# Kernel tuning notes

Measured on AMD Instinct MI355X. Metric: run time of the kernel, lower is better.

The kernel has to match this reference:

```python
import jax, jax.numpy as jnp
import numpy as np


def _conv(x, w, padding):
    # x: NCHW, w: OIHW
    return jax.lax.conv_general_dilated(
        x, w, window_strides=(1, 1), padding=padding,
        dimension_numbers=('NCHW', 'OIHW', 'NCHW'))


def setup_inputs() -> dict:
    key = jax.random.key(0)
    ks = jax.random.split(key, 4)
    B, Cin, H, W = 128, 1024, 14, 14
    planes, expansion = 256, 4
    x = jax.random.normal(ks[0], (B, Cin, H, W), dtype=jnp.float32)
    # conv weights (layouts are fully dense since rho=0.0)
    w1 = jax.random.normal(ks[1], (planes, Cin, 1, 1), dtype=jnp.float32) * 0.02
    w2 = jax.random.normal(ks[2], (planes, planes, 3, 3), dtype=jnp.float32) * 0.02
    w3 = jax.random.normal(ks[3], (planes * expansion, planes, 1, 1), dtype=jnp.float32) * 0.02
    # Fixup scalar biases / scale
    z = jnp.zeros((1,), dtype=jnp.float32)
    return {
        'x': x, 'w1': w1, 'w2': w2, 'w3': w3,
        'bias1b': z, 'bias2a': z, 'bias2b': z, 'bias3a': z, 'bias3b': z,
        'rscale': jnp.ones((1,), dtype=jnp.float32), 'rbias': z,
    }


def reference(x, w1, w2, w3, bias1b, bias2a, bias2b, bias3a, bias3b, rscale, rbias):
    # conv1(x) + bias1b  (1x1, fused output bias)
    out = _conv(x, w1, 'VALID') + bias1b[0]
    # conv2(out + bias2a) + bias2b  (3x3, pad 1, fused input+output bias)
    out = _conv(out + bias2a[0], w2, 'SAME') + bias2b[0]
    # conv3(out + bias3a) + bias3b  (1x1)
    out = _conv(out + bias3a[0], w3, 'VALID') + bias3b[0]
    # fused scale + bias + residual ReLU: relu(out*rscale + rbias + identity)
    return jax.nn.relu(out * rscale[0] + rbias[0] + x)
```

## Files before the change

kernel.cpp:

```cpp
#include <hip/hip_runtime.h>
#include <stdint.h>

typedef __bf16 bf16x8 __attribute__((ext_vector_type(8)));
typedef float f32x4 __attribute__((ext_vector_type(4)));
typedef unsigned short u16;

__device__ __forceinline__ u16 f2bf(float f){
  uint32_t u = __float_as_uint(f);
  u = (u + 0x7fffu + ((u >> 16) & 1u)) >> 16;
  return (u16)u;
}
__device__ __forceinline__ float bf2f(u16 v){
  return __uint_as_float(((uint32_t)v) << 16);
}
__device__ __forceinline__ void gl_lds16(const void* g, void* l){
  __builtin_amdgcn_global_load_lds((const __attribute__((address_space(1))) void*)g,
                                   (__attribute__((address_space(3))) void*)l, 16, 0, 0);
}

__global__ __launch_bounds__(256) void prep_all(
    const float* __restrict__ w1, const float* __restrict__ w2,
    const float* __restrict__ w3, u16* __restrict__ wb1, u16* __restrict__ wb2,
    u16* __restrict__ wb3, u16* __restrict__ xp1){
  int bid = blockIdx.x, t = threadIdx.x;
  if (bid < 1024){
    int i = bid*256 + t; wb1[i] = f2bf(w1[i]);
  } else if (bid < 3328){
    int i = (bid-1024)*256 + t;
    int o = i / 2304, r = i - o*2304, kq = r >> 8, c = r & 255;
    wb2[i] = f2bf(w2[((size_t)o*256 + c)*9 + kq]);
  } else if (bid < 4352){
    int i = (bid-3328)*256 + t; wb3[i] = f2bf(w3[i]);
  } else {
    int tid = (bid-4352)*256 + t;
    int row_i = tid >> 5, w = tid & 31;
    unsigned b = (unsigned)row_i / 60u, k = (unsigned)row_i - b*60u;
    int y, xx;
    if (k < 32){ y = (k>>4)*15; xx = k & 15; }
    else if (k < 46){ y = k - 31; xx = 0; }
    else { y = k - 45; xx = 15; }
    size_t row = (size_t)b*256 + y*16 + xx;
    ((ulonglong2*)(xp1 + row*256))[w] = (ulonglong2){0,0};
  }
}

__global__ __launch_bounds__(256) void transform_x(const float* __restrict__ x,
                                                   u16* __restrict__ xp0){
  __shared__ float lds[64*201];
  const int b = blockIdx.y, c0 = blockIdx.x*64, t = threadIdx.x;
  const float4* src = (const float4*)x + (size_t)b*50176 + (size_t)c0*49;
  #pragma unroll
  for (int r = 0; r < 13; ++r){
    int q = r*256 + t;
    if (q < 3136){
      unsigned c = (unsigned)q / 49u, f = (unsigned)q - c*49u;
      float4 v = src[q];
      float* d = &lds[c*201 + f*4];
      d[0]=v.x; d[1]=v.y; d[2]=v.z; d[3]=v.w;
    }
  }
  __syncthreads();
  const int c4 = (t & 15)*4, pg = t >> 4;
  #pragma unroll
  for (int r = 0; r < 13; ++r){
    int p = r*16 + pg;
    if (p < 196){
      ushort4 pk;
      ((u16*)&pk)[0] = f2bf(lds[(c4+0)*201 + p]);
      ((u16*)&pk)[1] = f2bf(lds[(c4+1)*201 + p]);
      ((u16*)&pk)[2] = f2bf(lds[(c4+2)*201 + p]);
      ((u16*)&pk)[3] = f2bf(lds[(c4+3)*201 + p]);
      *(ushort4*)&xp0[((size_t)b*196 + p)*1024 + c0 + c4] = pk;
    }
  }
}

template<int CID>
__device__ __forceinline__ void gemm_body(
    const u16* __restrict__ A, const u16* __restrict__ B,
    u16* __restrict__ Obf, float* __restrict__ Of32, const u16* __restrict__ xresb,
    const float* __restrict__ s0, const float* __restrict__ s1, const float* __restrict__ s2)
{
  constexpr int KTOT  = (CID==1) ? 1024 : (CID==2) ? 2304 : 256;
  constexpr int NSTEP = KTOT / 64;
  constexpr int BN    = (CID==3) ? 128 : 64;
  constexpr int WN    = (CID==3) ? 64 : 32;
  constexpr int NJ    = WN / 16;
  constexpr int NBG   = BN*8/256;
  constexpr int BUFB  = 16384 + BN*128;
  constexpr int LDSZ  = (CID==3) ? 33792 : 2*BUFB;

  __shared__ char lds[LDSZ];
  const int t    = threadIdx.x;
  const int lane = t & 63;
  const int w    = t >> 6;
  const int wm   = (w >> 1) * 64, wn = (w & 1) * WN;

  const int orig = blockIdx.x;
  const int bid  = (orig & 7) * ((int)gridDim.x >> 3) + (orig >> 3);
  int n0, m0;
  if constexpr (CID==3){ n0 = (bid >> 3) * 128; m0 = (bid & 7) * 128; }
  else                 { n0 = (bid >> 1) * 64;  m0 = (bid & 1) * 128; }

  f32x4 acc[4][NJ] = {};

  uint32_t aoff[4], boff[NBG];
  #pragma unroll
  for (int i = 0; i < 4; ++i){
    int gl = i*256 + t, row = gl >> 3, ss = gl & 7;
    int xo = (ss ^ (row & 7)) << 4;
    aoff[i] = (uint32_t)(m0 + row) * (KTOT*2) + xo;
  }
  #pragma unroll
  for (int i = 0; i < NBG; ++i){
    int gl = i*256 + t, row = gl >> 3, ss = gl & 7;
    int xo = (ss ^ (row & 7)) << 4;
    uint32_t n = n0 + row;
    if constexpr (CID==1)      boff[i] = n * 2048u + xo;
    else if constexpr (CID==3) boff[i] = n * 512u + xo;
    else {
      uint32_t b = n / 196u, p = n - b*196u;
      uint32_t py = p / 14u,  px = p - py*14u;
      uint32_t prow = b*256u + (py+1)*16u + (px+1);
      boff[i] = prow * 512u + xo;
    }
  }

  auto stage = [&](int buf, int s){
    char* Ab = lds + buf*BUFB;
    char* Bb = Ab + 16384;
    const int ka = s*128;
    int kb;
    if constexpr (CID==2){
      int kq = s >> 2;
      kb = ((kq/3 - 1)*16 + (kq%3) - 1)*512 + (s & 3)*128;
    } else kb = ka;
    #pragma unroll
    for (int i = 0; i < 4; ++i)
      gl_lds16((const char*)A + aoff[i] + ka, Ab + (i*256 + t)*16);
    #pragma unroll
    for (int i = 0; i < NBG; ++i)
      gl_lds16((const char*)B + (int64_t)boff[i] + kb, Bb + (i*256 + t)*16);
  };

  auto compute = [&](int buf){
    char* Ab = lds + buf*BUFB;
    char* Bb = Ab + 16384;
    #pragma unroll
    for (int h = 0; h < 2; ++h){
      bf16x8 af[4], bfr[NJ];
      #pragma unroll
      for (int i = 0; i < 4; ++i){
        int row = wm + i*16 + (lane & 15);
        af[i] = *(const bf16x8*)(Ab + row*128 + (((h*4 + (lane>>4)) ^ (row & 7)) << 4));
      }
      #pragma unroll
      for (int j = 0; j < NJ; ++j){
        int row = wn + j*16 + (lane & 15);
        bfr[j] = *(const bf16x8*)(Bb + row*128 + (((h*4 + (lane>>4)) ^ (row & 7)) << 4));
      }
      #pragma unroll
      for (int i = 0; i < 4; ++i)
        #pragma unroll
        for (int j = 0; j < NJ; ++j)
          acc[i][j] = __builtin_amdgcn_mfma_f32_16x16x32_bf16(af[i], bfr[j], acc[i][j], 0, 0, 0);
    }
  };

  if constexpr (CID==3){
    #pragma unroll
    for (int s = 0; s < NSTEP; ++s){
      if (s) __syncthreads();
      stage(0, s);
      __syncthreads();
      compute(0);
    }
  } else {
    stage(0, 0);
    __syncthreads();
    for (int s = 0; s < NSTEP; ++s){
      if (s + 1 < NSTEP) stage((s+1) & 1, s+1);
      compute(s & 1);
      __syncthreads();
    }
  }

  if constexpr (CID==1 || CID==2){
    float badd = s0[0] + s1[0];
    #pragma unroll
    for (int i = 0; i < 4; ++i){
      int o = m0 + wm + i*16 + ((lane >> 4) << 2);
      #pragma unroll
      for (int j = 0; j < NJ; ++j){
        uint32_t n = n0 + wn + j*16 + (lane & 15);
        size_t rn;
        if constexpr (CID==1){
          uint32_t b = n / 196u, p = n - b*196u;
          uint32_t py = p / 14u, px = p - py*14u;
          rn = (size_t)b*256 + (py+1)*16 + (px+1);
        } else rn = n;
        ushort4 pk;
        #pragma unroll
        for (int q = 0; q < 4; ++q) ((u16*)&pk)[q] = f2bf(acc[i][j][q] + badd);
        *(ushort4*)(Obf + rn*256 + o) = pk;
      }
    }
  } else {
    float b3 = s0[0], rs = s1[0], rbv = s2[0];
    float* ldsF = (float*)lds;
    #pragma unroll
    for (int pass = 0; pass < 2; ++pass){
      __syncthreads();
      if ((wm >> 6) == pass){
        #pragma unroll
        for (int i = 0; i < 4; ++i){
          int rb = i*16 + ((lane >> 4) << 2);
          #pragma unroll
          for (int j = 0; j < 4; ++j){
            int col = wn + j*16 + (lane & 15);
            #pragma unroll
            for (int q = 0; q < 4; ++q) ldsF[(rb + q)*132 + col] = acc[i][j][q];
          }
        }
      }
      __syncthreads();
      #pragma unroll
      for (int r = 0; r < 8; ++r){
        int row = (w << 4) + ((lane >> 5) << 3) + r;
        int n4  = (lane & 31) << 2;
        float4 v = *(float4*)&ldsF[row*132 + n4];
        uint32_t n = n0 + n4;
        uint32_t b = n / 196u, p = n - b*196u;
        int o = m0 + pass*64 + row;
        size_t base = ((size_t)b*1024 + o)*196 + p;
        const u16* xr = xresb + (size_t)n*1024 + o;
        float4 ov;
        ov.x = fmaxf((v.x + b3)*rs + rbv + bf2f(xr[0]),    0.f);
        ov.y = fmaxf((v.y + b3)*rs + rbv + bf2f(xr[1024]), 0.f);
        ov.z = fmaxf((v.z + b3)*rs + rbv + bf2f(xr[2048]), 0.f);
        ov.w = fmaxf((v.w + b3)*rs + rbv + bf2f(xr[3072]), 0.f);
        *(float4*)&Of32[base] = ov;
      }
    }
  }
}

__global__ __launch_bounds__(256, 3) void gemm1_conv(
    const u16* __restrict__ A, const u16* __restrict__ B, u16* __restrict__ O,
    const float* __restrict__ s0, const float* __restrict__ s1){
  gemm_body<1>(A, B, O, nullptr, nullptr, s0, s1, nullptr);
}
__global__ __launch_bounds__(256, 3) void gemm2_conv(
    const u16* __restrict__ A, const u16* __restrict__ B, u16* __restrict__ O,
    const float* __restrict__ s0, const float* __restrict__ s1){
  gemm_body<2>(A, B, O, nullptr, nullptr, s0, s1, nullptr);
}
__global__ __launch_bounds__(256, 4) void gemm3_conv(
    const u16* __restrict__ A, const u16* __restrict__ B, const u16* __restrict__ xresb,
    float* __restrict__ O, const float* __restrict__ s0, const float* __restrict__ s1,
    const float* __restrict__ s2){
  gemm_body<3>(A, B, nullptr, O, xresb, s0, s1, s2);
}

extern "C" void kernel_launch(void* const* d_in, const int* in_sizes, int n_in,
                              void* d_out, int out_size, void* d_ws, size_t ws_size,
                              hipStream_t stream){
  (void)in_sizes; (void)n_in; (void)out_size; (void)ws_size;
  const float* x   = (const float*)d_in[0];
  const float* w1  = (const float*)d_in[1];
  const float* w2  = (const float*)d_in[2];
  const float* w3  = (const float*)d_in[3];
  const float* b1b = (const float*)d_in[4];
  const float* b2a = (const float*)d_in[5];
  const float* b2b = (const float*)d_in[6];
  const float* b3a = (const float*)d_in[7];
  const float* b3b = (const float*)d_in[8];
  const float* rsc = (const float*)d_in[9];
  const float* rbi = (const float*)d_in[10];

  char* ws  = (char*)d_ws;
  u16*  xp1 = (u16*)ws;
  u16*  xp2 = (u16*)(ws + 16777216);
  u16*  xp0 = (u16*)(ws + 29622272);
  u16*  wb1 = (u16*)(ws + 81002496);
  u16*  wb2 = (u16*)(ws + 81526784);
  u16*  wb3 = (u16*)(ws + 82706432);

  prep_all   <<<dim3(5312),   256, 0, stream>>>(w1, w2, w3, wb1, wb2, wb3, xp1);
  transform_x<<<dim3(16,128), 256, 0, stream>>>(x, xp0);

  gemm1_conv<<<dim3(784),  256, 0, stream>>>(wb1, xp0, xp1, b1b, b2a);
  gemm2_conv<<<dim3(784),  256, 0, stream>>>(wb2, xp1, xp2, b2b, b3a);
  gemm3_conv<<<dim3(1568), 256, 0, stream>>>(wb3, xp2, xp0, (float*)d_out, b3b, rsc, rbi);
}
```

Baseline: 331.9 us.

## Restructure conv1/conv2 GEMMs as per-image padded-grid tiles with shared halo reuse

Conv1 and conv2 now run as 512-thread blocks that each own one image and 128 output channels, computing over the full padded 16x16 grid (256 columns). Conv1 writes zeros into the padding border itself, so the separate halo-zeroing pass in the prep kernel is removed. Conv2 loads one padded-image B tile per K chunk into LDS and reuses it for all nine 3x3 taps through row shifts, instead of re-gathering B for every tap. This cuts global B traffic and address math, in exchange for large dynamic LDS (about 100 KB), one block per CU, only 256 blocks, and wasted MMA work on padding positions.

```diff
diff --git a/kernel.cpp b/kernel.cpp
--- a/kernel.cpp
+++ b/kernel.cpp
@@ -18,10 +18,10 @@
                                    (__attribute__((address_space(3))) void*)l, 16, 0, 0);
 }
 
-__global__ __launch_bounds__(256) void prep_all(
+__global__ __launch_bounds__(256) void prep_w(
     const float* __restrict__ w1, const float* __restrict__ w2,
     const float* __restrict__ w3, u16* __restrict__ wb1, u16* __restrict__ wb2,
-    u16* __restrict__ wb3, u16* __restrict__ xp1){
+    u16* __restrict__ wb3){
   int bid = blockIdx.x, t = threadIdx.x;
   if (bid < 1024){
     int i = bid*256 + t; wb1[i] = f2bf(w1[i]);
@@ -29,18 +29,8 @@
     int i = (bid-1024)*256 + t;
     int o = i / 2304, r = i - o*2304, kq = r >> 8, c = r & 255;
     wb2[i] = f2bf(w2[((size_t)o*256 + c)*9 + kq]);
-  } else if (bid < 4352){
+  } else {
     int i = (bid-3328)*256 + t; wb3[i] = f2bf(w3[i]);
-  } else {
-    int tid = (bid-4352)*256 + t;
-    int row_i = tid >> 5, w = tid & 31;
-    unsigned b = (unsigned)row_i / 60u, k = (unsigned)row_i - b*60u;
-    int y, xx;
-    if (k < 32){ y = (k>>4)*15; xx = k & 15; }
-    else if (k < 46){ y = k - 31; xx = 0; }
-    else { y = k - 45; xx = 15; }
-    size_t row = (size_t)b*256 + y*16 + xx;
-    ((ulonglong2*)(xp1 + row*256))[w] = (ulonglong2){0,0};
   }
 }
 
@@ -75,191 +65,285 @@
   }
 }
 
-template<int CID>
-__device__ __forceinline__ void gemm_body(
-    const u16* __restrict__ A, const u16* __restrict__ B,
-    u16* __restrict__ Obf, float* __restrict__ Of32, const u16* __restrict__ xresb,
-    const float* __restrict__ s0, const float* __restrict__ s1, const float* __restrict__ s2)
-{
-  constexpr int KTOT  = (CID==1) ? 1024 : (CID==2) ? 2304 : 256;
-  constexpr int NSTEP = KTOT / 64;
-  constexpr int BN    = (CID==3) ? 128 : 64;
-  constexpr int WN    = (CID==3) ? 64 : 32;
-  constexpr int NJ    = WN / 16;
-  constexpr int NBG   = BN*8/256;
-  constexpr int BUFB  = 16384 + BN*128;
-  constexpr int LDSZ  = (CID==3) ? 33792 : 2*BUFB;
-
-  __shared__ char lds[LDSZ];
-  const int t    = threadIdx.x;
-  const int lane = t & 63;
-  const int w    = t >> 6;
-  const int wm   = (w >> 1) * 64, wn = (w & 1) * WN;
-
+__global__ __launch_bounds__(512, 1) void gemm1_conv(
+    const u16* __restrict__ A, const u16* __restrict__ B, u16* __restrict__ O,
+    const float* __restrict__ s0, const float* __restrict__ s1){
+  extern __shared__ char lds[];
+  const int t = threadIdx.x, lane = t & 63, w = t >> 6;
+  const int wm = (w >> 2) * 64, wn = (w & 3) * 64;
+  const int b = blockIdx.x & 127, m0 = (blockIdx.x >> 7) * 128;
+  f32x4 acc[4][4] = {};
+
+  uint32_t aoff[2], boff[4];
+  #pragma unroll
+  for (int i = 0; i < 2; ++i){
+    int gl = i*512 + t, row = gl >> 3, ss = gl & 7;
+    aoff[i] = (uint32_t)(m0 + row)*2048 + ((ss ^ (row & 7)) << 4);
+  }
+  #pragma unroll
+  for (int i = 0; i < 4; ++i){
+    int gl = i*512 + t, row = gl >> 3, ss = gl & 7;
+    int y = row >> 4, x = row & 15;
+    int p = ((unsigned)(y-1) < 14u && (unsigned)(x-1) < 14u) ? (y-1)*14 + (x-1) : 0;
+    boff[i] = ((uint32_t)b*196 + p)*2048 + ((ss ^ (row & 7)) << 4);
+  }
+
+  auto stage = [&](int buf, int kc){
+    char* Ab = lds + buf*16384;
+    char* Bb = lds + 32768 + buf*32768;
+    #pragma unroll
+    for (int i = 0; i < 2; ++i)
+      gl_lds16((const char*)A + aoff[i] + kc*128, Ab + (i*512 + t)*16);
+    #pragma unroll
+    for (int i = 0; i < 4; ++i)
+      gl_lds16((const char*)B + boff[i] + kc*128, Bb + (i*512 + t)*16);
+  };
+  auto compute = [&](int buf){
+    char* Ab = lds + buf*16384;
+    char* Bb = lds + 32768 + buf*32768;
+    #pragma unroll
+    for (int h = 0; h < 2; ++h){
+      bf16x8 af[4], bfr[4];
+      #pragma unroll
+      for (int i = 0; i < 4; ++i){
+        int row = wm + i*16 + (lane & 15);
+        af[i] = *(const bf16x8*)(Ab + row*128 + (((h*4 + (lane>>4)) ^ (row & 7)) << 4));
+      }
+      #pragma unroll
+      for (int j = 0; j < 4; ++j){
+        int row = wn + j*16 + (lane & 15);
+        bfr[j] = *(const bf16x8*)(Bb + row*128 + (((h*4 + (lane>>4)) ^ (row & 7)) << 4));
+      }
+      #pragma unroll
+      for (int i = 0; i < 4; ++i)
+        #pragma unroll
+        for (int j = 0; j < 4; ++j)
+          acc[i][j] = __builtin_amdgcn_mfma_f32_16x16x32_bf16(af[i], bfr[j], acc[i][j], 0, 0, 0);
+    }
+  };
+
+  stage(0, 0);
+  __syncthreads();
+  #pragma unroll
+  for (int kc = 0; kc < 16; ++kc){
+    if (kc < 15) stage((kc+1) & 1, kc+1);
+    compute(kc & 1);
+    __syncthreads();
+  }
+
+  float badd = s0[0] + s1[0];
+  #pragma unroll
+  for (int i = 0; i < 4; ++i){
+    int o = m0 + wm + i*16 + ((lane >> 4) << 2);
+    #pragma unroll
+    for (int j = 0; j < 4; ++j){
+      int n = wn + j*16 + (lane & 15);
+      int y = n >> 4, x = n & 15;
+      bool real = ((unsigned)(y-1) < 14u) && ((unsigned)(x-1) < 14u);
+      ushort4 pk;
+      #pragma unroll
+      for (int q = 0; q < 4; ++q)
+        ((u16*)&pk)[q] = real ? f2bf(acc[i][j][q] + badd) : (u16)0;
+      *(ushort4*)(O + ((size_t)b*256 + n)*256 + o) = pk;
+    }
+  }
+}
+
+__global__ __launch_bounds__(512, 1) void gemm2_conv(
+    const u16* __restrict__ A, const u16* __restrict__ B, u16* __restrict__ O,
+    const float* __restrict__ s0, const float* __restrict__ s1){
+  extern __shared__ char lds[];
+  const int t = threadIdx.x, lane = t & 63, w = t >> 6;
+  const int wm = (w >> 2) * 64, wn = (w & 3) * 64;
+  const int b = blockIdx.x & 127, m0 = (blockIdx.x >> 7) * 128;
+  f32x4 acc[4][4] = {};
+
+  uint32_t aoff[2], boff[5];
+  #pragma unroll
+  for (int i = 0; i < 2; ++i){
+    int gl = i*512 + t, row = gl >> 3, ss = gl & 7;
+    aoff[i] = (uint32_t)(m0 + row)*4608 + ((ss ^ (row & 7)) << 4);
+  }
+  #pragma unroll
+  for (int i = 0; i < 5; ++i){
+    int gl = i*512 + t, row = gl >> 3, ss = gl & 7;
+    int pos = row - 18;
+    pos = pos < 0 ? 0 : (pos > 255 ? 255 : pos);
+    boff[i] = ((uint32_t)b*256 + pos)*512 + ((ss ^ (row & 7)) << 4);
+  }
+
+  auto stageA = [&](int buf, int kq, int kc){
+    char* Ab = lds + buf*16384;
+    int off = kq*512 + kc*128;
+    #pragma unroll
+    for (int i = 0; i < 2; ++i)
+      gl_lds16((const char*)A + aoff[i] + off, Ab + (i*512 + t)*16);
+  };
+  auto stageB = [&](int buf, int kc){
+    char* Bb = lds + 32768 + buf*37376;
+    #pragma unroll
+    for (int i = 0; i < 5; ++i){
+      int gl = i*512 + t;
+      if (gl < 2336) gl_lds16((const char*)B + boff[i] + kc*128, Bb + gl*16);
+    }
+  };
+  auto compute = [&](int ab, int bb, int shift){
+    char* Ab = lds + ab*16384;
+    char* Bb = lds + 32768 + bb*37376;
+    #pragma unroll
+    for (int h = 0; h < 2; ++h){
+      bf16x8 af[4], bfr[4];
+      #pragma unroll
+      for (int i = 0; i < 4; ++i){
+        int row = wm + i*16 + (lane & 15);
+        af[i] = *(const bf16x8*)(Ab + row*128 + (((h*4 + (lane>>4)) ^ (row & 7)) << 4));
+      }
+      #pragma unroll
+      for (int j = 0; j < 4; ++j){
+        int row = 18 + wn + j*16 + (lane & 15) + shift;
+        bfr[j] = *(const bf16x8*)(Bb + row*128 + (((h*4 + (lane>>4)) ^ (row & 7)) << 4));
+      }
+      #pragma unroll
+      for (int i = 0; i < 4; ++i)
+        #pragma unroll
+        for (int j = 0; j < 4; ++j)
+          acc[i][j] = __builtin_amdgcn_mfma_f32_16x16x32_bf16(af[i], bfr[j], acc[i][j], 0, 0, 0);
+    }
+  };
+
+  stageB(0, 0); stageA(0, 0, 0);
+  __syncthreads();
+  int ab = 0, bbuf = 0;
+  #pragma unroll
+  for (int kc = 0; kc < 4; ++kc){
+    #pragma unroll
+    for (int kq = 0; kq < 9; ++kq){
+      if (kq < 8) stageA(ab ^ 1, kq + 1, kc);
+      else if (kc < 3){ stageB(bbuf ^ 1, kc + 1); stageA(ab ^ 1, 0, kc + 1); }
+      compute(ab, bbuf, (kq/3 - 1)*16 + (kq%3) - 1);
+      __syncthreads();
+      ab ^= 1;
+      if (kq == 8) bbuf ^= 1;
+    }
+  }
+
+  float badd = s0[0] + s1[0];
+  #pragma unroll
+  for (int i = 0; i < 4; ++i){
+    int o = m0 + wm + i*16 + ((lane >> 4) << 2);
+    #pragma unroll
+    for (int j = 0; j < 4; ++j){
+      int n = wn + j*16 + (lane & 15);
+      int y = n >> 4, x = n & 15;
+      if (((unsigned)(y-1) < 14u) && ((unsigned)(x-1) < 14u)){
+        int p = (y-1)*14 + (x-1);
+        ushort4 pk;
+        #pragma unroll
+        for (int q = 0; q < 4; ++q) ((u16*)&pk)[q] = f2bf(acc[i][j][q] + badd);
+        *(ushort4*)(O + ((size_t)b*196 + p)*256 + o) = pk;
+      }
+    }
+  }
+}
+
+__global__ __launch_bounds__(256, 4) void gemm3_conv(
+    const u16* __restrict__ A, const u16* __restrict__ B, const u16* __restrict__ xresb,
+    float* __restrict__ Of32, const float* __restrict__ s0, const float* __restrict__ s1,
+    const float* __restrict__ s2){
+  __shared__ char lds[33792];
+  const int t = threadIdx.x, lane = t & 63, w = t >> 6;
+  const int wm = (w >> 1) * 64, wn = (w & 1) * 64;
   const int orig = blockIdx.x;
   const int bid  = (orig & 7) * ((int)gridDim.x >> 3) + (orig >> 3);
-  int n0, m0;
-  if constexpr (CID==3){ n0 = (bid >> 3) * 128; m0 = (bid & 7) * 128; }
-  else                 { n0 = (bid >> 1) * 64;  m0 = (bid & 1) * 128; }
-
-  f32x4 acc[4][NJ] = {};
-
-  uint32_t aoff[4], boff[NBG];
+  const int n0 = (bid >> 3) * 128, m0 = (bid & 7) * 128;
+  f32x4 acc[4][4] = {};
+
+  uint32_t aoff[4], boff[4];
   #pragma unroll
   for (int i = 0; i < 4; ++i){
     int gl = i*256 + t, row = gl >> 3, ss = gl & 7;
     int xo = (ss ^ (row & 7)) << 4;
-    aoff[i] = (uint32_t)(m0 + row) * (KTOT*2) + xo;
-  }
-  #pragma unroll
-  for (int i = 0; i < NBG; ++i){
-    int gl = i*256 + t, row = gl >> 3, ss = gl & 7;
-    int xo = (ss ^ (row & 7)) << 4;
-    uint32_t n = n0 + row;
-    if constexpr (CID==1)      boff[i] = n * 2048u + xo;
-    else if constexpr (CID==3) boff[i] = n * 512u + xo;
-    else {
-      uint32_t b = n / 196u, p = n - b*196u;
-      uint32_t py = p / 14u,  px = p - py*14u;
-      uint32_t prow = b*256u + (py+1)*16u + (px+1);
-      boff[i] = prow * 512u + xo;
-    }
-  }
-
-  auto stage = [&](int buf, int s){
-    char* Ab = lds + buf*BUFB;
-    char* Bb = Ab + 16384;
-    const int ka = s*128;
-    int kb;
-    if constexpr (CID==2){
-      int kq = s >> 2;
-      kb = ((kq/3 - 1)*16 + (kq%3) - 1)*512 + (s & 3)*128;
-    } else kb = ka;
-    #pragma unroll
-    for (int i = 0; i < 4; ++i)
-      gl_lds16((const char*)A + aoff[i] + ka, Ab + (i*256 + t)*16);
-    #pragma unroll
-    for (int i = 0; i < NBG; ++i)
-      gl_lds16((const char*)B + (int64_t)boff[i] + kb, Bb + (i*256 + t)*16);
-  };
-
-  auto compute = [&](int buf){
-    char* Ab = lds + buf*BUFB;
-    char* Bb = Ab + 16384;
+    aoff[i] = (uint32_t)(m0 + row)*512 + xo;
+    boff[i] = (uint32_t)(n0 + row)*512 + xo;
+  }
+
+  auto stage = [&](int s){
+    char* Ab = lds;
+    char* Bb = lds + 16384;
+    #pragma unroll
+    for (int i = 0; i < 4; ++i){
+      gl_lds16((const char*)A + aoff[i] + s*128, Ab + (i*256 + t)*16);
+      gl_lds16((const char*)B + boff[i] + s*128, Bb + (i*256 + t)*16);
+    }
+  };
+  auto compute = [&](){
+    char* Ab = lds;
+    char* Bb = lds + 16384;
     #pragma unroll
     for (int h = 0; h < 2; ++h){
-      bf16x8 af[4], bfr[NJ];
+      bf16x8 af[4], bfr[4];
       #pragma unroll
       for (int i = 0; i < 4; ++i){
         int row = wm + i*16 + (lane & 15);
         af[i] = *(const bf16x8*)(Ab + row*128 + (((h*4 + (lane>>4)) ^ (row & 7)) << 4));
       }
       #pragma unroll
-      for (int j = 0; j < NJ; ++j){
+      for (int j = 0; j < 4; ++j){
         int row = wn + j*16 + (lane & 15);
         bfr[j] = *(const bf16x8*)(Bb + row*128 + (((h*4 + (lane>>4)) ^ (row & 7)) << 4));
       }
       #pragma unroll
       for (int i = 0; i < 4; ++i)
         #pragma unroll
-        for (int j = 0; j < NJ; ++j)
+        for (int j = 0; j < 4; ++j)
           acc[i][j] = __builtin_amdgcn_mfma_f32_16x16x32_bf16(af[i], bfr[j], acc[i][j], 0, 0, 0);
     }
   };
 
-  if constexpr (CID==3){
-    #pragma unroll
-    for (int s = 0; s < NSTEP; ++s){
-      if (s) __syncthreads();
-      stage(0, s);
-      __syncthreads();
-      compute(0);
-    }
-  } else {
-    stage(0, 0);
+  #pragma unroll
+  for (int s = 0; s < 4; ++s){
+    if (s) __syncthreads();
+    stage(s);
     __syncthreads();
-    for (int s = 0; s < NSTEP; ++s){
-      if (s + 1 < NSTEP) stage((s+1) & 1, s+1);
-      compute(s & 1);
-      __syncthreads();
-    }
-  }
-
-  if constexpr (CID==1 || CID==2){
-    float badd = s0[0] + s1[0];
-    #pragma unroll
-    for (int i = 0; i < 4; ++i){
-      int o = m0 + wm + i*16 + ((lane >> 4) << 2);
-      #pragma unroll
-      for (int j = 0; j < NJ; ++j){
-        uint32_t n = n0 + wn + j*16 + (lane & 15);
-        size_t rn;
-        if constexpr (CID==1){
-          uint32_t b = n / 196u, p = n - b*196u;
-          uint32_t py = p / 14u, px = p - py*14u;
-          rn = (size_t)b*256 + (py+1)*16 + (px+1);
-        } else rn = n;
-        ushort4 pk;
-        #pragma unroll
-        for (int q = 0; q < 4; ++q) ((u16*)&pk)[q] = f2bf(acc[i][j][q] + badd);
-        *(ushort4*)(Obf + rn*256 + o) = pk;
-      }
-    }
-  } else {
-    float b3 = s0[0], rs = s1[0], rbv = s2[0];
-    float* ldsF = (float*)lds;
-    #pragma unroll
-    for (int pass = 0; pass < 2; ++pass){
-      __syncthreads();
-      if ((wm >> 6) == pass){
-        #pragma unroll
-        for (int i = 0; i < 4; ++i){
-          int rb = i*16 + ((lane >> 4) << 2);
+    compute();
+  }
+
+  float b3 = s0[0], rs = s1[0], rbv = s2[0];
+  float* ldsF = (float*)lds;
+  #pragma unroll
+  for (int pass = 0; pass < 2; ++pass){
+    __syncthreads();
+    if ((wm >> 6) == pass){
+      #pragma unroll
+      for (int i = 0; i < 4; ++i){
+        int rb = i*16 + ((lane >> 4) << 2);
+        #pragma unroll
+        for (int j = 0; j < 4; ++j){
+          int col = wn + j*16 + (lane & 15);
           #pragma unroll
-          for (int j = 0; j < 4; ++j){
-            int col = wn + j*16 + (lane & 15);
-            #pragma unroll
-            for (int q = 0; q < 4; ++q) ldsF[(rb + q)*132 + col] = acc[i][j][q];
-          }
+          for (int q = 0; q < 4; ++q) ldsF[(rb + q)*132 + col] = acc[i][j][q];
         }
       }
-      __syncthreads();
-      #pragma unroll
-      for (int r = 0; r < 8; ++r){
-        int row = (w << 4) + ((lane >> 5) << 3) + r;
-        int n4  = (lane & 31) << 2;
-        float4 v = *(float4*)&ldsF[row*132 + n4];
-        uint32_t n = n0 + n4;
-        uint32_t b = n / 196u, p = n - b*196u;
-        int o = m0 + pass*64 + row;
-        size_t base = ((size_t)b*1024 + o)*196 + p;
-        const u16* xr = xresb + (size_t)n*1024 + o;
-        float4 ov;
-        ov.x = fmaxf((v.x + b3)*rs + rbv + bf2f(xr[0]),    0.f);
-        ov.y = fmaxf((v.y + b3)*rs + rbv + bf2f(xr[1024]), 0.f);
-        ov.z = fmaxf((v.z + b3)*rs + rbv + bf2f(xr[2048]), 0.f);
-        ov.w = fmaxf((v.w + b3)*rs + rbv + bf2f(xr[3072]), 0.f);
-        *(float4*)&Of32[base] = ov;
-      }
-    }
-  }
-}
-
-__global__ __launch_bounds__(256, 3) void gemm1_conv(
-    const u16* __restrict__ A, const u16* __restrict__ B, u16* __restrict__ O,
-    const float* __restrict__ s0, const float* __restrict__ s1){
-  gemm_body<1>(A, B, O, nullptr, nullptr, s0, s1, nullptr);
-}
-__global__ __launch_bounds__(256, 3) void gemm2_conv(
-    const u16* __restrict__ A, const u16* __restrict__ B, u16* __restrict__ O,
-    const float* __restrict__ s0, const float* __restrict__ s1){
-  gemm_body<2>(A, B, O, nullptr, nullptr, s0, s1, nullptr);
-}
-__global__ __launch_bounds__(256, 4) void gemm3_conv(
-    const u16* __restrict__ A, const u16* __restrict__ B, const u16* __restrict__ xresb,
-    float* __restrict__ O, const float* __restrict__ s0, const float* __restrict__ s1,
-    const float* __restrict__ s2){
-  gemm_body<3>(A, B, nullptr, O, xresb, s0, s1, s2);
+    }
+    __syncthreads();
+    #pragma unroll
+    for (int r = 0; r < 8; ++r){
+      int row = (w << 4) + ((lane >> 5) << 3) + r;
+      int n4  = (lane & 31) << 2;
+      float4 v = *(float4*)&ldsF[row*132 + n4];
+      uint32_t n = n0 + n4;
+      uint32_t b = n / 196u, p = n - b*196u;
+      int o = m0 + pass*64 + row;
+      size_t base = ((size_t)b*1024 + o)*196 + p;
+      const u16* xr = xresb + (size_t)n*1024 + o;
+      float4 ov;
+      ov.x = fmaxf((v.x + b3)*rs + rbv + bf2f(xr[0]),    0.f);
+      ov.y = fmaxf((v.y + b3)*rs + rbv + bf2f(xr[1024]), 0.f);
+      ov.z = fmaxf((v.z + b3)*rs + rbv + bf2f(xr[2048]), 0.f);
+      ov.w = fmaxf((v.w + b3)*rs + rbv + bf2f(xr[3072]), 0.f);
+      *(float4*)&Of32[base] = ov;
+    }
+  }
 }
 
 extern "C" void kernel_launch(void* const* d_in, const int* in_sizes, int n_in,
@@ -286,10 +370,10 @@
   u16*  wb2 = (u16*)(ws + 81526784);
   u16*  wb3 = (u16*)(ws + 82706432);
 
-  prep_all   <<<dim3(5312),   256, 0, stream>>>(w1, w2, w3, wb1, wb2, wb3, xp1);
+  prep_w     <<<dim3(4352),   256, 0, stream>>>(w1, w2, w3, wb1, wb2, wb3);
   transform_x<<<dim3(16,128), 256, 0, stream>>>(x, xp0);
 
-  gemm1_conv<<<dim3(784),  256, 0, stream>>>(wb1, xp0, xp1, b1b, b2a);
-  gemm2_conv<<<dim3(784),  256, 0, stream>>>(wb2, xp1, xp2, b2b, b3a);
-  gemm3_conv<<<dim3(1568), 256, 0, stream>>>(wb3, xp2, xp0, (float*)d_out, b3b, rsc, rbi);
-}
+  gemm1_conv<<<dim3(256),  512,  98304, stream>>>(wb1, xp0, xp1, b1b, b2a);
+  gemm2_conv<<<dim3(256),  512, 107520, stream>>>(wb2, xp1, xp2, b2b, b3a);
+  gemm3_conv<<<dim3(1568), 256,      0, stream>>>(wb3, xp2, xp0, (float*)d_out, b3b, rsc, rbi);
+}
```

New measurement: 320.0 us. -3.6%, faster.
